# Optimization experiments

Measured on AMD Instinct MI355X. Metric: run time of the kernel, lower is better.

The kernel has to match this reference:

```python
import jax, jax.numpy as jnp
import numpy as np

SIGMA = 1.0


def _rbf_gram(A, B):
    # A: (Tb, N, C), B: (Tb, M, C) -> (Tb, N, M)
    AA = jnp.sum(A * A, axis=2, keepdims=True)          # (Tb, N, 1)
    BB = jnp.sum(B * B, axis=2, keepdims=True)          # (Tb, M, 1)
    d = AA + jnp.swapaxes(BB, 1, 2) - 2.0 * jnp.einsum('bnc,bmc->bnm', A, B)
    return jnp.exp(-d / (2.0 * SIGMA ** 2))


def setup_inputs() -> dict:
    key = jax.random.key(0)
    kx, ky = jax.random.split(key)
    x = jax.random.normal(kx, (512, 128, 16), dtype=jnp.float32)
    y = jax.random.normal(ky, (512, 128, 16), dtype=jnp.float32)
    return {"x": x, "y": y}


def reference(x, y):
    # x, y: (batch, stream, channel)
    x_fds = jnp.concatenate((x[:, :-1, :], x[:, 1:, :]), axis=1)  # (B, 2(T-1), C)
    y_fds = jnp.concatenate((y[:, :-1, :], y[:, 1:, :]), axis=1)
    xf = jnp.transpose(x_fds, (1, 0, 2))  # (2(T-1), B, C)
    yf = jnp.transpose(y_fds, (1, 0, 2))

    N = xf.shape[1]
    Kxx = _rbf_gram(xf, xf)  # (2(T-1), N, N)
    # off-diagonal mean per batch: (sum - trace) / (N*(N-1))
    e_xx = (Kxx.sum(axis=(1, 2)) - jnp.trace(Kxx, axis1=1, axis2=2)) / (N * (N - 1))
    E_k_x1_x2 = e_xx.mean()

    Kxy = _rbf_gram(xf, yf)
    E_k_x_y = Kxy.mean(axis=(1, 2)).mean()

    return E_k_x1_x2 - 2.0 * E_k_x_y
```

## Files before the change

kernel.cpp:

```cpp
#include <hip/hip_runtime.h>


#define LOG2E 1.4426950408889634f
#define SCALE 1.2011224087864498f

typedef __attribute__((ext_vector_type(8))) __bf16 bf16x8;
typedef __attribute__((ext_vector_type(4))) float floatx4;

union FragU { uint4 q; unsigned int u[4]; bf16x8 v; };

static __device__ __forceinline__ int off(int n) { return (n << 3) + ((n >> 2) << 2); }

static __device__ __forceinline__ unsigned short bfbits(__bf16 h) {
    union { __bf16 h; unsigned short s; } u; u.h = h; return u.s;
}
static __device__ __forceinline__ unsigned int packhh(__bf16 a, __bf16 b) {
    return (unsigned int)bfbits(a) | ((unsigned int)bfbits(b) << 16);
}

#define NSLOT 26

__global__ __launch_bounds__(256, 8) void mmd_kernel(const float* __restrict__ x,
                                                     const float* __restrict__ y,
                                                     float* __restrict__ part) {
    __shared__ unsigned int AH[1152], AL[1152], BH[1152], BL[1152];
    __shared__ float csB[128], srg[128];
    __shared__ float red[4];

    const int slot = blockIdx.x;
    const int t    = blockIdx.y;
    const int tid  = threadIdx.x;
    const int w    = tid >> 6;
    const int lane = tid & 63;
    const int quad = lane >> 4;
    const int l15  = lane & 15;
    const int qh   = quad & 1;

    int sa, sq, isxx;
    if (slot < 16) { isxx = 0; sa = slot >> 2; sq = slot & 3; }
    else {
        isxx = 1;
        const int s = slot - 16;
        if      (s < 4) { sa = 0; sq = s; }
        else if (s < 7) { sa = 1; sq = s - 3; }
        else if (s < 9) { sa = 2; sq = s - 5; }
        else            { sa = 3; sq = 3; }
    }

    {
        const int half = tid >> 7;
        const int r    = tid & 127;
        const int grow = (half ? sq : sa) * 128 + r;
        const float4* __restrict__ src4 =
            (half && !isxx) ? (const float4*)y : (const float4*)x;
        const size_t gb = (size_t)grow * 512 + t * 4;
        float4 f0 = src4[gb], f1 = src4[gb + 1], f2 = src4[gb + 2], f3 = src4[gb + 3];
        const float fs[16] = { f0.x, f0.y, f0.z, f0.w, f1.x, f1.y, f1.z, f1.w,
                               f2.x, f2.y, f2.z, f2.w, f3.x, f3.y, f3.z, f3.w };
        float g = 0.f;
        unsigned int hw[8], lw[8];
#pragma unroll
        for (int p = 0; p < 8; ++p) {
            const float v0 = fs[2 * p], v1 = fs[2 * p + 1];
            g += v0 * v0 + v1 * v1;
            const float s0 = v0 * SCALE, s1 = v1 * SCALE;
            const __bf16 h0 = (__bf16)s0, h1 = (__bf16)s1;
            hw[p] = packhh(h0, h1);
            lw[p] = packhh((__bf16)(s0 - (float)h0), (__bf16)(s1 - (float)h1));
        }
        const float gp = 0.5f * LOG2E * g;
        unsigned int* __restrict__ H = half ? BH : AH;
        unsigned int* __restrict__ L = half ? BL : AL;
        const int o = off(r);
        *(uint4*)&H[o]     = make_uint4(hw[0], hw[1], hw[2], hw[3]);
        *(uint4*)&H[o + 4] = make_uint4(hw[4], hw[5], hw[6], hw[7]);
        *(uint4*)&L[o]     = make_uint4(lw[0], lw[1], lw[2], lw[3]);
        *(uint4*)&L[o + 4] = make_uint4(lw[4], lw[5], lw[6], lw[7]);
        if (half) csB[r] = __builtin_amdgcn_exp2f(-gp);
        else      srg[r] = gp;
    }
    __syncthreads();

    bf16x8 a1f[2], a2f[2];
    {
        FragU z; z.q = make_uint4(0u, 0u, 0u, 0u);
#pragma unroll
        for (int rt = 0; rt < 2; ++rt) {
            const int row = w * 32 + rt * 16 + l15;
            const int rb  = off(row) + qh * 4;
            FragU u;
            u.q = (quad < 2) ? *(const uint4*)&AH[rb] : *(const uint4*)&AL[rb];
            a1f[rt] = u.v;
            a2f[rt] = (quad < 2) ? u.v : z.v;
        }
    }

    float sum[2][4] = {{0.f, 0.f, 0.f, 0.f}, {0.f, 0.f, 0.f, 0.f}};

    floatx4 accP[2], accC[2];
    float csP;
    {
        const int rb = off(l15) + qh * 4;
        FragU bh, bl;
        bh.q = *(const uint4*)&BH[rb];
        bl.q = *(const uint4*)&BL[rb];
        csP = csB[l15];
        floatx4 zc = {0.f, 0.f, 0.f, 0.f};
        accP[0] = __builtin_amdgcn_mfma_f32_16x16x32_bf16(a1f[0], bh.v, zc, 0, 0, 0);
        accP[0] = __builtin_amdgcn_mfma_f32_16x16x32_bf16(a2f[0], bl.v, accP[0], 0, 0, 0);
        accP[1] = __builtin_amdgcn_mfma_f32_16x16x32_bf16(a1f[1], bh.v, zc, 0, 0, 0);
        accP[1] = __builtin_amdgcn_mfma_f32_16x16x32_bf16(a2f[1], bl.v, accP[1], 0, 0, 0);
    }
#pragma unroll
    for (int jt = 1; jt < 8; ++jt) {
        const int n  = jt * 16 + l15;
        const int rb = off(n) + qh * 4;
        FragU bh, bl;
        bh.q = *(const uint4*)&BH[rb];
        bl.q = *(const uint4*)&BL[rb];
        const float cs = csB[n];
        floatx4 zc = {0.f, 0.f, 0.f, 0.f};
        accC[0] = __builtin_amdgcn_mfma_f32_16x16x32_bf16(a1f[0], bh.v, zc, 0, 0, 0);
        accC[0] = __builtin_amdgcn_mfma_f32_16x16x32_bf16(a2f[0], bl.v, accC[0], 0, 0, 0);
        accC[1] = __builtin_amdgcn_mfma_f32_16x16x32_bf16(a1f[1], bh.v, zc, 0, 0, 0);
        accC[1] = __builtin_amdgcn_mfma_f32_16x16x32_bf16(a2f[1], bl.v, accC[1], 0, 0, 0);
#pragma unroll
        for (int rt = 0; rt < 2; ++rt)
#pragma unroll
            for (int r = 0; r < 4; ++r)
                sum[rt][r] = fmaf(__builtin_amdgcn_exp2f(accP[rt][r]), csP, sum[rt][r]);
        accP[0] = accC[0];
        accP[1] = accC[1];
        csP = cs;
    }
#pragma unroll
    for (int rt = 0; rt < 2; ++rt)
#pragma unroll
        for (int r = 0; r < 4; ++r)
            sum[rt][r] = fmaf(__builtin_amdgcn_exp2f(accP[rt][r]), csP, sum[rt][r]);

    float tot = 0.f;
#pragma unroll
    for (int rt = 0; rt < 2; ++rt)
#pragma unroll
        for (int r = 0; r < 4; ++r) {
            const float rs = __builtin_amdgcn_exp2f(-srg[w * 32 + rt * 16 + quad * 4 + r]);
            tot = fmaf(sum[rt][r], rs, tot);
        }
    for (int o = 32; o > 0; o >>= 1) tot += __shfl_down(tot, o, 64);
    if (lane == 0) red[w] = tot;
    __syncthreads();
    if (tid == 0) {
        float wt = (t == 0 || t == 127) ? 1.f : 2.f;
        if (isxx && sq > sa) wt *= 2.f;
        const int idx = isxx ? (2048 + t * 10 + (slot - 16)) : (t * 16 + slot);
        part[idx] = wt * (red[0] + red[1] + red[2] + red[3]);
    }
}

__global__ __launch_bounds__(256) void finalize_kernel(const float* __restrict__ part,
                                                       float* __restrict__ out) {
    const int tid = threadIdx.x;
    double vxy = 0.0, vxx = 0.0;
#pragma unroll
    for (int k = 0; k < 8; ++k)  vxy += (double)part[tid + 256 * k];
#pragma unroll
    for (int k = 8; k < 13; ++k) vxx += (double)part[tid + 256 * k];
    for (int o = 32; o > 0; o >>= 1) {
        vxx += __shfl_down(vxx, o, 64);
        vxy += __shfl_down(vxy, o, 64);
    }
    __shared__ double red[8];
    const int wid = tid >> 6;
    if ((tid & 63) == 0) { red[wid] = vxx; red[4 + wid] = vxy; }
    __syncthreads();
    if (tid == 0) {
        double sxx = red[0] + red[1] + red[2] + red[3];
        double sxy = red[4] + red[5] + red[6] + red[7];
        double e1 = (sxx - 254.0 * 512.0) / (254.0 * 512.0 * 511.0);
        double e2 = sxy / (254.0 * 512.0 * 512.0);
        out[0] = (float)(e1 - 2.0 * e2);
    }
}

extern "C" void kernel_launch(void* const* d_in, const int* in_sizes, int n_in,
                              void* d_out, int out_size, void* d_ws, size_t ws_size,
                              hipStream_t stream) {
    (void)in_sizes; (void)n_in; (void)out_size; (void)ws_size;
    const float* x = (const float*)d_in[0];
    const float* y = (const float*)d_in[1];
    float* out  = (float*)d_out;
    float* part = (float*)d_ws;

    mmd_kernel<<<dim3(NSLOT, 128), dim3(256), 0, stream>>>(x, y, part);
    finalize_kernel<<<dim3(1), dim3(256), 0, stream>>>(part, out);
}
```

Before: 74.47 us.

## Drop bf16 lo-split, fold column norm bias into MFMA K-padding

Removes the hi/lo bf16 split of the scaled inputs, so each tile uses one MFMA instead of two and half the LDS traffic. The per-column -|b|^2 term is packed as a bf16 hi+lo pair into the unused K lanes (quad 2), paired with ones in the A fragment, so the MFMA output already includes the bias and the exp2 result no longer needs a multiply by a column scale. Inputs are now rounded to single bf16, which lowers dot-product precision and may affect accuracy.

```diff
diff --git a/kernel.cpp b/kernel.cpp
--- a/kernel.cpp
+++ b/kernel.cpp
@@ -19,12 +19,15 @@
 }
 
 #define NSLOT 26
+#define ONEONE 0x3F803F80u
 
 __global__ __launch_bounds__(256, 8) void mmd_kernel(const float* __restrict__ x,
                                                      const float* __restrict__ y,
                                                      float* __restrict__ part) {
-    __shared__ unsigned int AH[1152], AL[1152], BH[1152], BL[1152];
-    __shared__ float csB[128], srg[128];
+    __shared__ unsigned int AH[1152], BH[1152];
+    __shared__ unsigned int BG[512];
+    __shared__ float srg[128];
+    __shared__ unsigned int zero4[4];
     __shared__ float red[4];
 
     const int slot = blockIdx.x;
@@ -47,6 +50,8 @@
         else            { sa = 3; sq = 3; }
     }
 
+    if (tid == 0) { zero4[0] = 0u; zero4[1] = 0u; zero4[2] = 0u; zero4[3] = 0u; }
+
     {
         const int half = tid >> 7;
         const int r    = tid & 127;
@@ -58,86 +63,77 @@
         const float fs[16] = { f0.x, f0.y, f0.z, f0.w, f1.x, f1.y, f1.z, f1.w,
                                f2.x, f2.y, f2.z, f2.w, f3.x, f3.y, f3.z, f3.w };
         float g = 0.f;
-        unsigned int hw[8], lw[8];
+        unsigned int hw[8];
 #pragma unroll
         for (int p = 0; p < 8; ++p) {
             const float v0 = fs[2 * p], v1 = fs[2 * p + 1];
             g += v0 * v0 + v1 * v1;
-            const float s0 = v0 * SCALE, s1 = v1 * SCALE;
-            const __bf16 h0 = (__bf16)s0, h1 = (__bf16)s1;
-            hw[p] = packhh(h0, h1);
-            lw[p] = packhh((__bf16)(s0 - (float)h0), (__bf16)(s1 - (float)h1));
+            hw[p] = packhh((__bf16)(v0 * SCALE), (__bf16)(v1 * SCALE));
         }
         const float gp = 0.5f * LOG2E * g;
         unsigned int* __restrict__ H = half ? BH : AH;
-        unsigned int* __restrict__ L = half ? BL : AL;
         const int o = off(r);
         *(uint4*)&H[o]     = make_uint4(hw[0], hw[1], hw[2], hw[3]);
         *(uint4*)&H[o + 4] = make_uint4(hw[4], hw[5], hw[6], hw[7]);
-        *(uint4*)&L[o]     = make_uint4(lw[0], lw[1], lw[2], lw[3]);
-        *(uint4*)&L[o + 4] = make_uint4(lw[4], lw[5], lw[6], lw[7]);
-        if (half) csB[r] = __builtin_amdgcn_exp2f(-gp);
-        else      srg[r] = gp;
+        if (half) {
+            const __bf16 nh = (__bf16)(-gp);
+            const __bf16 nl = (__bf16)(-(gp + (float)nh));
+            *(uint4*)&BG[r * 4] = make_uint4(packhh(nh, nl), 0u, 0u, 0u);
+        } else {
+            srg[r] = gp;
+        }
     }
     __syncthreads();
 
-    bf16x8 a1f[2], a2f[2];
+    bf16x8 a1f[2];
     {
-        FragU z; z.q = make_uint4(0u, 0u, 0u, 0u);
 #pragma unroll
         for (int rt = 0; rt < 2; ++rt) {
-            const int row = w * 32 + rt * 16 + l15;
-            const int rb  = off(row) + qh * 4;
             FragU u;
-            u.q = (quad < 2) ? *(const uint4*)&AH[rb] : *(const uint4*)&AL[rb];
+            if (quad < 2) {
+                const int row = w * 32 + rt * 16 + l15;
+                u.q = *(const uint4*)&AH[off(row) + qh * 4];
+            } else {
+                u.q = make_uint4((quad == 2) ? ONEONE : 0u, 0u, 0u, 0u);
+            }
             a1f[rt] = u.v;
-            a2f[rt] = (quad < 2) ? u.v : z.v;
         }
     }
+
+    const unsigned int* bptr;
+    int bstride;
+    if (quad < 2)      { bptr = &BH[off(l15) + qh * 4]; bstride = 144; }
+    else if (quad == 2){ bptr = &BG[l15 * 4];           bstride = 64;  }
+    else               { bptr = &zero4[0];              bstride = 0;   }
 
     float sum[2][4] = {{0.f, 0.f, 0.f, 0.f}, {0.f, 0.f, 0.f, 0.f}};
 
     floatx4 accP[2], accC[2];
-    float csP;
     {
-        const int rb = off(l15) + qh * 4;
-        FragU bh, bl;
-        bh.q = *(const uint4*)&BH[rb];
-        bl.q = *(const uint4*)&BL[rb];
-        csP = csB[l15];
+        FragU b; b.q = *(const uint4*)bptr; bptr += bstride;
         floatx4 zc = {0.f, 0.f, 0.f, 0.f};
-        accP[0] = __builtin_amdgcn_mfma_f32_16x16x32_bf16(a1f[0], bh.v, zc, 0, 0, 0);
-        accP[0] = __builtin_amdgcn_mfma_f32_16x16x32_bf16(a2f[0], bl.v, accP[0], 0, 0, 0);
-        accP[1] = __builtin_amdgcn_mfma_f32_16x16x32_bf16(a1f[1], bh.v, zc, 0, 0, 0);
-        accP[1] = __builtin_amdgcn_mfma_f32_16x16x32_bf16(a2f[1], bl.v, accP[1], 0, 0, 0);
+        accP[0] = __builtin_amdgcn_mfma_f32_16x16x32_bf16(a1f[0], b.v, zc, 0, 0, 0);
+        accP[1] = __builtin_amdgcn_mfma_f32_16x16x32_bf16(a1f[1], b.v, zc, 0, 0, 0);
     }
 #pragma unroll
     for (int jt = 1; jt < 8; ++jt) {
-        const int n  = jt * 16 + l15;
-        const int rb = off(n) + qh * 4;
-        FragU bh, bl;
-        bh.q = *(const uint4*)&BH[rb];
-        bl.q = *(const uint4*)&BL[rb];
-        const float cs = csB[n];
+        FragU b; b.q = *(const uint4*)bptr; bptr += bstride;
         floatx4 zc = {0.f, 0.f, 0.f, 0.f};
-        accC[0] = __builtin_amdgcn_mfma_f32_16x16x32_bf16(a1f[0], bh.v, zc, 0, 0, 0);
-        accC[0] = __builtin_amdgcn_mfma_f32_16x16x32_bf16(a2f[0], bl.v, accC[0], 0, 0, 0);
-        accC[1] = __builtin_amdgcn_mfma_f32_16x16x32_bf16(a1f[1], bh.v, zc, 0, 0, 0);
-        accC[1] = __builtin_amdgcn_mfma_f32_16x16x32_bf16(a2f[1], bl.v, accC[1], 0, 0, 0);
+        accC[0] = __builtin_amdgcn_mfma_f32_16x16x32_bf16(a1f[0], b.v, zc, 0, 0, 0);
+        accC[1] = __builtin_amdgcn_mfma_f32_16x16x32_bf16(a1f[1], b.v, zc, 0, 0, 0);
 #pragma unroll
         for (int rt = 0; rt < 2; ++rt)
 #pragma unroll
             for (int r = 0; r < 4; ++r)
-                sum[rt][r] = fmaf(__builtin_amdgcn_exp2f(accP[rt][r]), csP, sum[rt][r]);
+                sum[rt][r] += __builtin_amdgcn_exp2f(accP[rt][r]);
         accP[0] = accC[0];
         accP[1] = accC[1];
-        csP = cs;
     }
 #pragma unroll
     for (int rt = 0; rt < 2; ++rt)
 #pragma unroll
         for (int r = 0; r < 4; ++r)
-            sum[rt][r] = fmaf(__builtin_amdgcn_exp2f(accP[rt][r]), csP, sum[rt][r]);
+            sum[rt][r] += __builtin_amdgcn_exp2f(accP[rt][r]);
 
     float tot = 0.f;
 #pragma unroll
```

Result: faster. 71.79 us (-3.6%).
